# Kernel optimization log

Hardware: AMD Instinct MI355X
Metric: run time of the kernel (lower is better)

Reference implementation:

```python
import jax, jax.numpy as jnp
import numpy as np

DELTA = 1.0
EPS = 1e-8  # torch CosineSimilarity eps


def setup_inputs() -> dict:
    key = jax.random.key(0)
    k1, k2, k3, k4 = jax.random.split(key, 4)
    N1, N2, D, C = 4096, 4096, 256, 16
    return {
        "mmd1": jax.random.normal(k1, (N1, D), dtype=jnp.float32),
        "mmd2": jax.random.normal(k2, (N2, D), dtype=jnp.float32),
        "label1": jax.random.randint(k3, (N1,), 0, C, dtype=jnp.int64),
        "label2": jax.random.randint(k4, (N2,), 0, C, dtype=jnp.int64),
    }


def reference(mmd1, mmd2, label1, label2):
    # Normalize rows with torch-style eps clamp: x / max(||x||, eps)
    n1 = mmd1 / jnp.maximum(jnp.linalg.norm(mmd1, axis=1, keepdims=True), EPS)
    n2 = mmd2 / jnp.maximum(jnp.linalg.norm(mmd2, axis=1, keepdims=True), EPS)
    cos = jnp.einsum("id,jd->ij", n1, n2)  # [N1, N2] pairwise cosine
    same = label1[:, None] == label2[None, :]  # [N1, N2] bool
    per_pair = jnp.where(same, jnp.maximum(DELTA - cos, 0.0), cos)
    return jnp.mean(per_pair)
```

## Files before the change

kernel.cpp:

```cpp
#include <hip/hip_runtime.h>
#include <hip/hip_bf16.h>
#include <cstdint>

#define N1 4096
#define N2 4096
#define DD 256
#define DELTA 1.0f
#define EPSN 1e-8f

#define BM 128
#define BN 128
#define BK 32

typedef __attribute__((ext_vector_type(8))) __bf16 bf16x8;
typedef __attribute__((ext_vector_type(4))) float f32x4;

typedef const __attribute__((address_space(1))) void* gptr_t;
typedef __attribute__((address_space(3))) void* lptr_t;

__global__ __launch_bounds__(256) void normalize_kernel(
    const float* __restrict__ mmd1, const float* __restrict__ mmd2,
    ushort* __restrict__ out1, ushort* __restrict__ out2,
    float* __restrict__ ws_sum)
{
    int row = blockIdx.x;
    const float* src;
    ushort* dst;
    if (row < N1) { src = mmd1 + (size_t)row * DD;        dst = out1 + (size_t)row * DD; }
    else          { src = mmd2 + (size_t)(row - N1) * DD; dst = out2 + (size_t)(row - N1) * DD; }

    int t = threadIdx.x;
    float x = src[t];
    float ss = x * x;
    #pragma unroll
    for (int off = 32; off; off >>= 1) ss += __shfl_down(ss, off, 64);
    __shared__ float wsum[4];
    int wid = t >> 6, lane = t & 63;
    if (lane == 0) wsum[wid] = ss;
    __syncthreads();
    float tot = wsum[0] + wsum[1] + wsum[2] + wsum[3];
    float scale = 1.0f / fmaxf(sqrtf(tot), EPSN);
    __hip_bfloat16 b = __float2bfloat16(x * scale);
    dst[t] = *reinterpret_cast<const ushort*>(&b);

    if (row == 0 && t == 0) ws_sum[0] = 0.0f;
}

__global__ __launch_bounds__(256) void cos_gemm_kernel(
    const ushort* __restrict__ A, const ushort* __restrict__ B,
    const int* __restrict__ lab1, const int* __restrict__ lab2,
    float* __restrict__ ws_sum)
{
    __shared__ __align__(16) ushort As[BM * BK];
    __shared__ __align__(16) ushort Bs[BN * BK];
    __shared__ int l1s[BM];
    __shared__ int l2s[BN];
    __shared__ float wredsum[4];

    const int row0 = blockIdx.y * BM;
    const int col0 = blockIdx.x * BN;
    const int t = threadIdx.x;
    const int lane = t & 63, wid = t >> 6;
    const int wr = wid >> 1, wc = wid & 1;

    if (t < BM) l1s[t] = lab1[row0 + t];
    else        l2s[t - BM] = lab2[col0 + (t - BM)];

    f32x4 acc[4][4] = {};

    for (int k0 = 0; k0 < DD; k0 += BK) {
        __syncthreads();
        #pragma unroll
        for (int it = 0; it < 2; ++it) {
            int t2 = t + it * 256;
            int r = t2 >> 2;
            int c = (t2 & 3) * 8;
            __builtin_amdgcn_global_load_lds(
                (gptr_t)(A + (size_t)(row0 + r) * DD + k0 + c),
                (lptr_t)(&As[r * BK + c]), 16, 0, 0);
            __builtin_amdgcn_global_load_lds(
                (gptr_t)(B + (size_t)(col0 + r) * DD + k0 + c),
                (lptr_t)(&Bs[r * BK + c]), 16, 0, 0);
        }
        __syncthreads();

        bf16x8 af[4], bfr[4];
        const int krow = (lane >> 4) * 8;
        const int rsel = lane & 15;
        #pragma unroll
        for (int m = 0; m < 4; ++m)
            af[m] = *reinterpret_cast<const bf16x8*>(&As[(wr * 64 + m * 16 + rsel) * BK + krow]);
        #pragma unroll
        for (int n = 0; n < 4; ++n)
            bfr[n] = *reinterpret_cast<const bf16x8*>(&Bs[(wc * 64 + n * 16 + rsel) * BK + krow]);
        #pragma unroll
        for (int m = 0; m < 4; ++m)
            #pragma unroll
            for (int n = 0; n < 4; ++n)
                acc[m][n] = __builtin_amdgcn_mfma_f32_16x16x32_bf16(af[m], bfr[n], acc[m][n], 0, 0, 0);
    }

    float lsum = 0.0f;
    const int csel = lane & 15;
    const int rbase = (lane >> 4) * 4;
    #pragma unroll
    for (int n = 0; n < 4; ++n) {
        int j = wc * 64 + n * 16 + csel;
        int l2 = l2s[j];
        #pragma unroll
        for (int m = 0; m < 4; ++m) {
            #pragma unroll
            for (int e = 0; e < 4; ++e) {
                int i = wr * 64 + m * 16 + rbase + e;
                float cosv = acc[m][n][e];
                float v = (l1s[i] == l2) ? fmaxf(DELTA - cosv, 0.0f) : cosv;
                lsum += v;
            }
        }
    }
    #pragma unroll
    for (int off = 32; off; off >>= 1) lsum += __shfl_down(lsum, off, 64);
    if (lane == 0) wredsum[wid] = lsum;
    __syncthreads();
    if (t == 0) atomicAdd(ws_sum, wredsum[0] + wredsum[1] + wredsum[2] + wredsum[3]);
}

__global__ void finalize_kernel(const float* __restrict__ ws_sum, float* __restrict__ out) {
    out[0] = ws_sum[0] * (1.0f / ((float)N1 * (float)N2));
}

extern "C" void kernel_launch(void* const* d_in, const int* in_sizes, int n_in,
                              void* d_out, int out_size, void* d_ws, size_t ws_size,
                              hipStream_t stream) {
    const float* mmd1 = (const float*)d_in[0];
    const float* mmd2 = (const float*)d_in[1];
    const int* lab1 = (const int*)d_in[2];
    const int* lab2 = (const int*)d_in[3];

    ushort* n1b = (ushort*)d_ws;
    ushort* n2b = n1b + (size_t)N1 * DD;
    float* ws_sum = (float*)((char*)d_ws + (size_t)(N1 + N2) * DD * 2);
    float* out = (float*)d_out;

    normalize_kernel<<<N1 + N2, 256, 0, stream>>>(mmd1, mmd2, n1b, n2b, ws_sum);
    cos_gemm_kernel<<<dim3(BN / 4, BM / 4) , 256, 0, stream>>>(n1b, n2b, lab1, lab2, ws_sum);
    finalize_kernel<<<1, 1, 0, stream>>>(ws_sum, out);
}
```

Measured before the change: 93.59 us.

## Replace pairwise cosine GEMM with per-class normalized-sum algebraic reduction

```diff
diff --git a/kernel.cpp b/kernel.cpp
--- a/kernel.cpp
+++ b/kernel.cpp
@@ -1,132 +1,117 @@
 #include <hip/hip_runtime.h>
-#include <hip/hip_bf16.h>
 #include <cstdint>
 
 #define N1 4096
 #define N2 4096
 #define DD 256
-#define DELTA 1.0f
+#define NCLS 16
 #define EPSN 1e-8f
 
-#define BM 128
-#define BN 128
-#define BK 32
+#define MAIN_BLOCKS 128
+#define ROWS_PER_BLOCK 64
 
-typedef __attribute__((ext_vector_type(8))) __bf16 bf16x8;
-typedef __attribute__((ext_vector_type(4))) float f32x4;
+#define ACC_DWORDS 8225
 
-typedef const __attribute__((address_space(1))) void* gptr_t;
-typedef __attribute__((address_space(3))) void* lptr_t;
-
-__global__ __launch_bounds__(256) void normalize_kernel(
-    const float* __restrict__ mmd1, const float* __restrict__ mmd2,
-    ushort* __restrict__ out1, ushort* __restrict__ out2,
-    float* __restrict__ ws_sum)
-{
-    int row = blockIdx.x;
-    const float* src;
-    ushort* dst;
-    if (row < N1) { src = mmd1 + (size_t)row * DD;        dst = out1 + (size_t)row * DD; }
-    else          { src = mmd2 + (size_t)(row - N1) * DD; dst = out2 + (size_t)(row - N1) * DD; }
-
-    int t = threadIdx.x;
-    float x = src[t];
-    float ss = x * x;
-    #pragma unroll
-    for (int off = 32; off; off >>= 1) ss += __shfl_down(ss, off, 64);
-    __shared__ float wsum[4];
-    int wid = t >> 6, lane = t & 63;
-    if (lane == 0) wsum[wid] = ss;
-    __syncthreads();
-    float tot = wsum[0] + wsum[1] + wsum[2] + wsum[3];
-    float scale = 1.0f / fmaxf(sqrtf(tot), EPSN);
-    __hip_bfloat16 b = __float2bfloat16(x * scale);
-    dst[t] = *reinterpret_cast<const ushort*>(&b);
-
-    if (row == 0 && t == 0) ws_sum[0] = 0.0f;
+__global__ __launch_bounds__(256) void init_kernel(unsigned int* __restrict__ acc) {
+    int idx = blockIdx.x * 256 + threadIdx.x;
+    if (idx < ACC_DWORDS) acc[idx] = 0u;
 }
 
-__global__ __launch_bounds__(256) void cos_gemm_kernel(
-    const ushort* __restrict__ A, const ushort* __restrict__ B,
+__global__ __launch_bounds__(256) void classsum_kernel(
+    const float* __restrict__ mmd1, const float* __restrict__ mmd2,
     const int* __restrict__ lab1, const int* __restrict__ lab2,
-    float* __restrict__ ws_sum)
+    float* __restrict__ ws_acc, float* __restrict__ out)
 {
-    __shared__ __align__(16) ushort As[BM * BK];
-    __shared__ __align__(16) ushort Bs[BN * BK];
-    __shared__ int l1s[BM];
-    __shared__ int l2s[BN];
-    __shared__ float wredsum[4];
+    __shared__ float part[NCLS * DD];
+    __shared__ int hist[NCLS];
+    __shared__ float wredS[4], wredA[4];
+    __shared__ int isLast;
 
-    const int row0 = blockIdx.y * BM;
-    const int col0 = blockIdx.x * BN;
+    float* cs1 = ws_acc;
+    float* cs2 = ws_acc + NCLS * DD;
+    int* cc1 = (int*)(ws_acc + 2 * NCLS * DD);
+    int* cc2 = cc1 + NCLS;
+    unsigned int* counter = (unsigned int*)(cc2 + NCLS);
+
     const int t = threadIdx.x;
     const int lane = t & 63, wid = t >> 6;
-    const int wr = wid >> 1, wc = wid & 1;
+    const int side = blockIdx.x >> 6;
+    const int lb = blockIdx.x & 63;
 
-    if (t < BM) l1s[t] = lab1[row0 + t];
-    else        l2s[t - BM] = lab2[col0 + (t - BM)];
+    #pragma unroll
+    for (int s = t; s < NCLS * DD; s += 256) part[s] = 0.0f;
+    if (t < NCLS) hist[t] = 0;
+    __syncthreads();
 
-    f32x4 acc[4][4] = {};
+    const float* srcbase = side ? mmd2 : mmd1;
+    const int* labbase = side ? lab2 : lab1;
+    const int row0 = lb * ROWS_PER_BLOCK + wid * 16;
 
-    for (int k0 = 0; k0 < DD; k0 += BK) {
+    #pragma unroll 2
+    for (int i = 0; i < 16; ++i) {
+        int row = row0 + i;
+        const float* src = srcbase + (size_t)row * DD;
+        float x0 = src[lane];
+        float x1 = src[lane + 64];
+        float x2 = src[lane + 128];
+        float x3 = src[lane + 192];
+        float ss = x0 * x0 + x1 * x1 + x2 * x2 + x3 * x3;
+        #pragma unroll
+        for (int off = 32; off; off >>= 1) ss += __shfl_xor(ss, off, 64);
+        float sc = 1.0f / fmaxf(sqrtf(ss), EPSN);
+        int lb_ = labbase[row];
+        float* prow = &part[lb_ * DD];
+        atomicAdd(&prow[lane],        x0 * sc);
+        atomicAdd(&prow[lane + 64],   x1 * sc);
+        atomicAdd(&prow[lane + 128],  x2 * sc);
+        atomicAdd(&prow[lane + 192],  x3 * sc);
+        if (lane == 0) atomicAdd(&hist[lb_], 1);
+    }
+    __syncthreads();
+
+    float* cs = side ? cs2 : cs1;
+    #pragma unroll
+    for (int s = t; s < NCLS * DD; s += 256) atomicAdd(&cs[s], part[s]);
+    if (t < NCLS) atomicAdd((side ? cc2 : cc1) + t, hist[t]);
+
+    __threadfence();
+    if (t == 0) {
+        unsigned int old = atomicAdd(counter, 1u);
+        isLast = (old == MAIN_BLOCKS - 1) ? 1 : 0;
+    }
+    __syncthreads();
+    if (!isLast) return;
+
+    {
+        int d = t;
+        float a1 = 0.0f, a2 = 0.0f, dsame = 0.0f;
+        #pragma unroll
+        for (int c = 0; c < NCLS; ++c) {
+            float s1 = atomicAdd(&cs1[c * DD + d], 0.0f);
+            float s2 = atomicAdd(&cs2[c * DD + d], 0.0f);
+            a1 += s1; a2 += s2; dsame += s1 * s2;
+        }
+        float dall = a1 * a2;
+        #pragma unroll
+        for (int off = 32; off; off >>= 1) {
+            dsame += __shfl_xor(dsame, off, 64);
+            dall  += __shfl_xor(dall,  off, 64);
+        }
+        if (lane == 0) { wredS[wid] = dsame; wredA[wid] = dall; }
         __syncthreads();
-        #pragma unroll
-        for (int it = 0; it < 2; ++it) {
-            int t2 = t + it * 256;
-            int r = t2 >> 2;
-            int c = (t2 & 3) * 8;
-            __builtin_amdgcn_global_load_lds(
-                (gptr_t)(A + (size_t)(row0 + r) * DD + k0 + c),
-                (lptr_t)(&As[r * BK + c]), 16, 0, 0);
-            __builtin_amdgcn_global_load_lds(
-                (gptr_t)(B + (size_t)(col0 + r) * DD + k0 + c),
-                (lptr_t)(&Bs[r * BK + c]), 16, 0, 0);
-        }
-        __syncthreads();
-
-        bf16x8 af[4], bfr[4];
-        const int krow = (lane >> 4) * 8;
-        const int rsel = lane & 15;
-        #pragma unroll
-        for (int m = 0; m < 4; ++m)
-            af[m] = *reinterpret_cast<const bf16x8*>(&As[(wr * 64 + m * 16 + rsel) * BK + krow]);
-        #pragma unroll
-        for (int n = 0; n < 4; ++n)
-            bfr[n] = *reinterpret_cast<const bf16x8*>(&Bs[(wc * 64 + n * 16 + rsel) * BK + krow]);
-        #pragma unroll
-        for (int m = 0; m < 4; ++m)
-            #pragma unroll
-            for (int n = 0; n < 4; ++n)
-                acc[m][n] = __builtin_amdgcn_mfma_f32_16x16x32_bf16(af[m], bfr[n], acc[m][n], 0, 0, 0);
-    }
-
-    float lsum = 0.0f;
-    const int csel = lane & 15;
-    const int rbase = (lane >> 4) * 4;
-    #pragma unroll
-    for (int n = 0; n < 4; ++n) {
-        int j = wc * 64 + n * 16 + csel;
-        int l2 = l2s[j];
-        #pragma unroll
-        for (int m = 0; m < 4; ++m) {
-            #pragma unroll
-            for (int e = 0; e < 4; ++e) {
-                int i = wr * 64 + m * 16 + rbase + e;
-                float cosv = acc[m][n][e];
-                float v = (l1s[i] == l2) ? fmaxf(DELTA - cosv, 0.0f) : cosv;
-                lsum += v;
+        if (t == 0) {
+            float Dsame = wredS[0] + wredS[1] + wredS[2] + wredS[3];
+            float Dall  = wredA[0] + wredA[1] + wredA[2] + wredA[3];
+            long long scount = 0;
+            for (int c = 0; c < NCLS; ++c) {
+                int c1 = atomicAdd(&cc1[c], 0);
+                int c2 = atomicAdd(&cc2[c], 0);
+                scount += (long long)c1 * (long long)c2;
             }
+            out[0] = ((float)scount + Dall - 2.0f * Dsame)
+                     * (1.0f / ((float)N1 * (float)N2));
         }
     }
-    #pragma unroll
-    for (int off = 32; off; off >>= 1) lsum += __shfl_down(lsum, off, 64);
-    if (lane == 0) wredsum[wid] = lsum;
-    __syncthreads();
-    if (t == 0) atomicAdd(ws_sum, wredsum[0] + wredsum[1] + wredsum[2] + wredsum[3]);
-}
-
-__global__ void finalize_kernel(const float* __restrict__ ws_sum, float* __restrict__ out) {
-    out[0] = ws_sum[0] * (1.0f / ((float)N1 * (float)N2));
 }
 
 extern "C" void kernel_launch(void* const* d_in, const int* in_sizes, int n_in,
@@ -137,12 +122,9 @@
     const int* lab1 = (const int*)d_in[2];
     const int* lab2 = (const int*)d_in[3];
 
-    ushort* n1b = (ushort*)d_ws;
-    ushort* n2b = n1b + (size_t)N1 * DD;
-    float* ws_sum = (float*)((char*)d_ws + (size_t)(N1 + N2) * DD * 2);
+    float* ws_acc = (float*)d_ws;
     float* out = (float*)d_out;
 
-    normalize_kernel<<<N1 + N2, 256, 0, stream>>>(mmd1, mmd2, n1b, n2b, ws_sum);
-    cos_gemm_kernel<<<dim3(BN / 4, BM / 4) , 256, 0, stream>>>(n1b, n2b, lab1, lab2, ws_sum);
-    finalize_kernel<<<1, 1, 0, stream>>>(ws_sum, out);
+    init_kernel<<<(ACC_DWORDS + 255) / 256, 256, 0, stream>>>((unsigned int*)ws_acc);
+    classsum_kernel<<<MAIN_BLOCKS, 256, 0, stream>>>(mmd1, mmd2, lab1, lab2, ws_acc, out);
 }
```

Measured after the change: 100.5 us. 7.3% more time.
